# Performance work log

Hardware: AMD Instinct MI355X
Metric: run time of the kernel (lower is better)

The kernel has to match this reference:

```python
import jax, jax.numpy as jnp
import numpy as np

EPS = 1e-7  # keras_backend.epsilon()
ROUTINGS = 3


def setup_inputs() -> dict:
    key = jax.random.key(0)
    k1, k2, k3, k4, k5 = jax.random.split(key, 5)
    B, H, W, I, O = 32, 8, 8, 32, 64
    return {
        "inputs_poses": jax.random.normal(k1, (B, H, W, I, 4, 4), dtype=jnp.float32),
        "inputs_activations": jax.random.uniform(k2, (B, H, W, I), dtype=jnp.float32),
        "w": jax.random.normal(k3, (I, O, 4, 4), dtype=jnp.float32),
        "beta_v": jax.random.normal(k4, (1, O), dtype=jnp.float32),
        "beta_a": jax.random.normal(k5, (1, O), dtype=jnp.float32),
    }


def _em_routing(votes, i_act, beta_v, beta_a, routings):
    # votes: [B, N, O, 16], i_act: [B, N]
    B, N, O, P = votes.shape
    act = i_act[..., None, None]              # [B, N, 1, 1]
    bv = beta_v[..., None, :, None]           # [1, 1, O, 1]
    ba = beta_a[..., None, :, None]           # [1, 1, O, 1]
    rr = jnp.full((N, O, 1), 1.0 / O, dtype=votes.dtype)
    it_min, it_max = 1.0, min(routings, 3.0)
    o_mean = o_act = None
    for it in range(routings):
        inv_temp = it_min + (it_max - it_min) * it / max(1.0, routings - 1.0)
        # ---- m-step ----
        rr_prime = rr * act                                    # [B, N, O, 1]
        rps = rr_prime.sum(axis=-3, keepdims=True)             # [B, 1, O, 1]
        o_mean = (rr_prime * votes).sum(axis=-3, keepdims=True) / rps   # [B,1,O,16]
        o_stdv = jnp.sqrt((rr_prime * jnp.square(votes - o_mean)).sum(axis=-3, keepdims=True) / rps)
        o_cost_h = (bv + jnp.log(o_stdv + EPS)) * rps          # [B,1,O,16]
        o_cost = o_cost_h.sum(axis=-1, keepdims=True)          # [B,1,O,1]
        o_cost_mean = o_cost.mean(axis=-2, keepdims=True)      # [B,1,1,1]
        o_cost_stdv = jnp.sqrt(jnp.square(o_cost - o_cost_mean).sum(axis=-2, keepdims=True) / O)
        o_act = jax.nn.sigmoid(inv_temp * (ba + (o_cost_mean - o_cost) / (o_cost_stdv + EPS)))
        # ---- e-step ----
        if it < routings - 1:
            o_p = (-jnp.sum(jnp.square(votes - o_mean) / (2.0 * jnp.square(o_stdv)), axis=-1, keepdims=True)
                   - jnp.sum(jnp.log(o_stdv + EPS), axis=-1, keepdims=True))   # [B,N,O,1]
            zz = jnp.log(o_act + EPS) + o_p
            rr = jax.nn.softmax(zz, axis=-2)                   # softmax over O
    poses = jnp.squeeze(o_mean, axis=-3)                       # [B, O, 16]
    activations = jnp.squeeze(o_act, axis=(-3, -1))            # [B, O]
    return poses, activations


def reference(inputs_poses, inputs_activations, w, beta_v, beta_a):
    B, H, W, I = inputs_activations.shape
    O = w.shape[1]
    # mat_transform: per-(input-type, class) 4x4 pose transform -> votes
    pose = inputs_poses.reshape(B * H * W, I, 4, 4)
    votes = jnp.einsum('siab,iobc->sioac', pose, w)            # [BHW, I, O, 4, 4]
    votes = votes.reshape(B, H, W, I, O, 16)
    # coord_addition: add scaled spatial coords to components 0 (h) and 1 (w)
    ch = jnp.zeros((1, H, 1, 1, 1, 16), votes.dtype).at[..., 0].set(
        ((jnp.arange(H, dtype=votes.dtype) + 0.5) / H).reshape(1, H, 1, 1, 1))
    cw = jnp.zeros((1, 1, W, 1, 1, 16), votes.dtype).at[..., 1].set(
        ((jnp.arange(W, dtype=votes.dtype) + 0.5) / W).reshape(1, 1, W, 1, 1))
    votes = votes + ch + cw
    votes = votes.reshape(B, H * W * I, O, 16)
    i_act = inputs_activations.reshape(B, H * W * I)
    poses, activations = _em_routing(votes, i_act, beta_v, beta_a, ROUTINGS)
    poses = poses.reshape(B, O, 4, 4)
    return poses, activations
```

## Files before the change

kernel.cpp:

```cpp
#include <hip/hip_runtime.h>
#include <hip/hip_bf16.h>


#define NB 32
#define NN 2048
#define NO 64
#define NP 16
#define EPSF 1e-7f

#define SPB 4
#define NCHUNK 16
#define BLK_N (SPB * 32)

#define ACC_SLOTS 33
#define ACC_PER_B (ACC_SLOTS * NO)
#define PART_TOTAL (NB * NCHUNK * ACC_PER_B)

template <bool FIRST>
__global__ __launch_bounds__(1024) void accum_kernel(
    const float* __restrict__ pose,
    const float* __restrict__ act,
    const float* __restrict__ wmat,
    const float* __restrict__ stats,
    float* __restrict__ part)
{
    __shared__ float pose_s[BLK_N * 16];
    __shared__ float act_s[BLK_N];
    __shared__ float buf[SPB][ACC_PER_B];

    const int b = blockIdx.y;
    const int chunk = blockIdx.x;
    const int n0 = chunk * BLK_N;
    const int tid = threadIdx.x;

    {
        const float4* psrc = (const float4*)(pose + ((size_t)b * NN + n0) * 16);
        float4* pdst = (float4*)pose_s;
        if (tid < BLK_N * 4) pdst[tid] = psrc[tid];
        if (tid < BLK_N) act_s[tid] = act[(size_t)b * NN + n0 + tid];
    }
    __syncthreads();

    const int wv = tid >> 6;
    const int grp = wv >> 2;
    const int wvin = wv & 3;
    const int o = tid & 63;

    float m[16], i2v[16], zzb = 0.f;
    if (!FIRST) {
        const float* st = stats + (size_t)b * ACC_PER_B;
        #pragma unroll
        for (int p = 0; p < 16; p++) m[p] = st[p * 64 + o];
        #pragma unroll
        for (int p = 0; p < 16; p++) i2v[p] = st[(16 + p) * 64 + o];
        zzb = st[32 * 64 + o];
    }

    float accR = 0.f, acc1[16], acc2[16];
    #pragma unroll
    for (int p = 0; p < 16; p++) { acc1[p] = 0.f; acc2[p] = 0.f; }

    const int site = chunk * SPB + grp;
    const int hh = site >> 3, ww = site & 7;
    const float c0 = (hh + 0.5f) * 0.125f;
    const float c1 = (ww + 0.5f) * 0.125f;

    for (int ii = 0; ii < 8; ii++) {
        const int i = wvin * 8 + ii;
        const int nl = grp * 32 + i;
        const float4* wp = (const float4*)(wmat + ((size_t)i * 64 + o) * 16);
        float4 w0 = wp[0], w1 = wp[1], w2 = wp[2], w3 = wp[3];
        const float* pr = pose_s + nl * 16;
        float v[16];
        #pragma unroll
        for (int a = 0; a < 4; a++) {
            float pa0 = pr[a * 4 + 0], pa1 = pr[a * 4 + 1];
            float pa2 = pr[a * 4 + 2], pa3 = pr[a * 4 + 3];
            v[a * 4 + 0] = pa0 * w0.x + pa1 * w1.x + pa2 * w2.x + pa3 * w3.x;
            v[a * 4 + 1] = pa0 * w0.y + pa1 * w1.y + pa2 * w2.y + pa3 * w3.y;
            v[a * 4 + 2] = pa0 * w0.z + pa1 * w1.z + pa2 * w2.z + pa3 * w3.z;
            v[a * 4 + 3] = pa0 * w0.w + pa1 * w1.w + pa2 * w2.w + pa3 * w3.w;
        }
        v[0] += c0;
        v[1] += c1;

        float rr;
        if (FIRST) {
            rr = 1.0f / 64.0f;
        } else {
            float d = zzb;
            #pragma unroll
            for (int p = 0; p < 16; p++) {
                float t = v[p] - m[p];
                d -= t * t * i2v[p];
            }
            float mx = d;
            #pragma unroll
            for (int s = 32; s > 0; s >>= 1) mx = fmaxf(mx, __shfl_xor(mx, s, 64));
            float e = __expf(d - mx);
            float sum = e;
            #pragma unroll
            for (int s = 32; s > 0; s >>= 1) sum += __shfl_xor(sum, s, 64);
            rr = e / sum;
        }
        float rp = rr * act_s[nl];
        accR += rp;
        #pragma unroll
        for (int p = 0; p < 16; p++) {
            acc1[p] += rp * v[p];
            acc2[p] += rp * v[p] * v[p];
        }
    }

    if (wvin == 3) {
        float* r = buf[grp];
        r[32 * 64 + o] = accR;
        #pragma unroll
        for (int p = 0; p < 16; p++) r[p * 64 + o] = acc1[p];
        #pragma unroll
        for (int p = 0; p < 16; p++) r[(16 + p) * 64 + o] = acc2[p];
    }
    __syncthreads();
    if (wvin == 2) {
        float* r = buf[grp];
        r[32 * 64 + o] += accR;
        #pragma unroll
        for (int p = 0; p < 16; p++) r[p * 64 + o] += acc1[p];
        #pragma unroll
        for (int p = 0; p < 16; p++) r[(16 + p) * 64 + o] += acc2[p];
    }
    __syncthreads();
    if (wvin == 1) {
        float* r = buf[grp];
        r[32 * 64 + o] += accR;
        #pragma unroll
        for (int p = 0; p < 16; p++) r[p * 64 + o] += acc1[p];
        #pragma unroll
        for (int p = 0; p < 16; p++) r[(16 + p) * 64 + o] += acc2[p];
    }
    __syncthreads();
    if (wvin == 0) {
        float* r = buf[grp];
        r[32 * 64 + o] += accR;
        #pragma unroll
        for (int p = 0; p < 16; p++) r[p * 64 + o] += acc1[p];
        #pragma unroll
        for (int p = 0; p < 16; p++) r[(16 + p) * 64 + o] += acc2[p];
    }
    __syncthreads();

    float* pc = part + ((size_t)b * NCHUNK + chunk) * ACC_PER_B;
    for (int j = tid; j < ACC_PER_B; j += 1024)
        pc[j] = buf[0][j] + buf[1][j] + buf[2][j] + buf[3][j];
}

__global__ __launch_bounds__(256) void stats_kernel(
    const float* __restrict__ part,
    const float* __restrict__ beta_v,
    const float* __restrict__ beta_a,
    float* __restrict__ stats_out,
    float* __restrict__ out,
    float inv_temp)
{
    __shared__ float acc_s[ACC_PER_B];

    const int b = blockIdx.x;
    const int tid = threadIdx.x;

    {
        const float4* p4 = (const float4*)(part + (size_t)b * NCHUNK * ACC_PER_B);
        float4* a4 = (float4*)acc_s;
        for (int j = tid; j < ACC_PER_B / 4; j += 256) {
            float4 s = make_float4(0.f, 0.f, 0.f, 0.f);
            #pragma unroll
            for (int c = 0; c < NCHUNK; c++) {
                float4 v = p4[c * (ACC_PER_B / 4) + j];
                s.x += v.x; s.y += v.y; s.z += v.z; s.w += v.w;
            }
            a4[j] = s;
        }
    }
    __syncthreads();

    if (tid < 64) {
        const int o = tid;
        float rps = acc_s[32 * 64 + o];
        float m[16], var[16];
        float logsum = 0.f;
        #pragma unroll
        for (int p = 0; p < 16; p++) {
            float s1 = acc_s[p * 64 + o];
            float s2 = acc_s[(16 + p) * 64 + o];
            float mm = s1 / rps;
            float vv = fmaxf(s2 / rps - mm * mm, 0.f);
            m[p] = mm;
            var[p] = vv;
            logsum += __logf(sqrtf(vv) + EPSF);
        }
        float cost = rps * (16.0f * beta_v[o] + logsum);

        float cm = cost;
        #pragma unroll
        for (int s = 32; s > 0; s >>= 1) cm += __shfl_xor(cm, s, 64);
        cm *= (1.0f / 64.0f);
        float d = cost - cm;
        float cs = d * d;
        #pragma unroll
        for (int s = 32; s > 0; s >>= 1) cs += __shfl_xor(cs, s, 64);
        cs = sqrtf(cs * (1.0f / 64.0f));

        float x = inv_temp * (beta_a[o] + (cm - cost) / (cs + EPSF));
        float oa = 1.0f / (1.0f + __expf(-x));

        if (stats_out) {
            float* st = stats_out + (size_t)b * ACC_PER_B;
            #pragma unroll
            for (int p = 0; p < 16; p++) st[p * 64 + o] = m[p];
            #pragma unroll
            for (int p = 0; p < 16; p++) st[(16 + p) * 64 + o] = 0.5f / var[p];
            st[32 * 64 + o] = __logf(oa + EPSF) - logsum;
        }
        if (out) {
            float* op = out + ((size_t)b * 64 + o) * 16;
            #pragma unroll
            for (int p = 0; p < 16; p++) op[p] = m[p];
            out[(size_t)NB * NO * NP + (size_t)b * 64 + o] = oa;
        }
    }
}

extern "C" void kernel_launch(void* const* d_in, const int* in_sizes, int n_in,
                              void* d_out, int out_size, void* d_ws, size_t ws_size,
                              hipStream_t stream) {
    const float* pose   = (const float*)d_in[0];
    const float* act    = (const float*)d_in[1];
    const float* wmat   = (const float*)d_in[2];
    const float* beta_v = (const float*)d_in[3];
    const float* beta_a = (const float*)d_in[4];
    float* out = (float*)d_out;
    float* ws = (float*)d_ws;

    float* part   = ws;
    float* stats0 = ws + (size_t)PART_TOTAL;
    float* stats1 = stats0 + (size_t)NB * ACC_PER_B;

    dim3 grid(NCHUNK, NB);
    accum_kernel<true><<<grid, 1024, 0, stream>>>(pose, act, wmat, nullptr, part);
    stats_kernel<<<NB, 256, 0, stream>>>(part, beta_v, beta_a, stats0, nullptr, 1.0f);
    accum_kernel<false><<<grid, 1024, 0, stream>>>(pose, act, wmat, stats0, part);
    stats_kernel<<<NB, 256, 0, stream>>>(part, beta_v, beta_a, stats1, nullptr, 2.0f);
    accum_kernel<false><<<grid, 1024, 0, stream>>>(pose, act, wmat, stats1, part);
    stats_kernel<<<NB, 256, 0, stream>>>(part, beta_v, beta_a, nullptr, out, 3.0f);
}
```

Before: 171.4 us.

## Fuse intermediate stats computation into accumulation kernels and read poses directly

Removes the two intermediate stats kernels by having each block of the next accumulation pass reduce the previous pass's per-chunk partials and compute the mean, inverse variance and log-activation terms itself. Partial sums now ping-pong between two workspace buffers. Pose and activation values are read straight from global memory with wave-uniform indices instead of being staged in shared memory first. This cuts two kernel launches and their serialization, but each of the 16 chunk blocks per batch now repeats the same partial reduction and stats math redundantly.

```diff
diff --git a/kernel.cpp b/kernel.cpp
--- a/kernel.cpp
+++ b/kernel.cpp
@@ -1,5 +1,4 @@
 #include <hip/hip_runtime.h>
-#include <hip/hip_bf16.h>
 
 
 #define NB 32
@@ -14,72 +13,141 @@
 
 #define ACC_SLOTS 33
 #define ACC_PER_B (ACC_SLOTS * NO)
-#define PART_TOTAL (NB * NCHUNK * ACC_PER_B)
+#define PART_PER_BATCH (NCHUNK * ACC_PER_B)
+#define PART_TOTAL (NB * PART_PER_BATCH)
+
+__device__ __forceinline__ void reduce_store(
+    float buf[SPB][ACC_PER_B], int wvin, int grp, int o, int tid,
+    float accR, const float* acc1, const float* acc2, float* __restrict__ pc)
+{
+    if (wvin == 3) {
+        float* r = buf[grp];
+        r[32 * 64 + o] = accR;
+        #pragma unroll
+        for (int p = 0; p < 16; p++) r[p * 64 + o] = acc1[p];
+        #pragma unroll
+        for (int p = 0; p < 16; p++) r[(16 + p) * 64 + o] = acc2[p];
+    }
+    __syncthreads();
+    for (int round = 2; round >= 0; --round) {
+        if (wvin == round) {
+            float* r = buf[grp];
+            r[32 * 64 + o] += accR;
+            #pragma unroll
+            for (int p = 0; p < 16; p++) r[p * 64 + o] += acc1[p];
+            #pragma unroll
+            for (int p = 0; p < 16; p++) r[(16 + p) * 64 + o] += acc2[p];
+        }
+        __syncthreads();
+    }
+    for (int j = tid; j < ACC_PER_B; j += 1024)
+        pc[j] = buf[0][j] + buf[1][j] + buf[2][j] + buf[3][j];
+}
 
 template <bool FIRST>
 __global__ __launch_bounds__(1024) void accum_kernel(
     const float* __restrict__ pose,
     const float* __restrict__ act,
     const float* __restrict__ wmat,
-    const float* __restrict__ stats,
-    float* __restrict__ part)
+    const float* __restrict__ beta_v,
+    const float* __restrict__ beta_a,
+    const float* __restrict__ part_prev,
+    float* __restrict__ part_out,
+    float inv_temp)
 {
-    __shared__ float pose_s[BLK_N * 16];
-    __shared__ float act_s[BLK_N];
     __shared__ float buf[SPB][ACC_PER_B];
 
     const int b = blockIdx.y;
     const int chunk = blockIdx.x;
     const int n0 = chunk * BLK_N;
     const int tid = threadIdx.x;
-
-    {
-        const float4* psrc = (const float4*)(pose + ((size_t)b * NN + n0) * 16);
-        float4* pdst = (float4*)pose_s;
-        if (tid < BLK_N * 4) pdst[tid] = psrc[tid];
-        if (tid < BLK_N) act_s[tid] = act[(size_t)b * NN + n0 + tid];
-    }
-    __syncthreads();
-
-    const int wv = tid >> 6;
-    const int grp = wv >> 2;
-    const int wvin = wv & 3;
-    const int o = tid & 63;
+    const int wv = tid >> 6, grp = wv >> 2, wvin = wv & 3, o = tid & 63;
 
     float m[16], i2v[16], zzb = 0.f;
     if (!FIRST) {
-        const float* st = stats + (size_t)b * ACC_PER_B;
-        #pragma unroll
-        for (int p = 0; p < 16; p++) m[p] = st[p * 64 + o];
-        #pragma unroll
-        for (int p = 0; p < 16; p++) i2v[p] = st[(16 + p) * 64 + o];
-        zzb = st[32 * 64 + o];
-    }
+        float* sb = buf[0];
+        {
+            const float4* p4 = (const float4*)(part_prev + (size_t)b * PART_PER_BATCH);
+            float4* a4 = (float4*)sb;
+            for (int j = tid; j < ACC_PER_B / 4; j += 1024) {
+                float4 s = make_float4(0.f, 0.f, 0.f, 0.f);
+                #pragma unroll
+                for (int c = 0; c < NCHUNK; c++) {
+                    float4 vv = p4[c * (ACC_PER_B / 4) + j];
+                    s.x += vv.x; s.y += vv.y; s.z += vv.z; s.w += vv.w;
+                }
+                a4[j] = s;
+            }
+        }
+        __syncthreads();
+        if (tid < 64) {
+            float rps = sb[32 * 64 + o];
+            float mm[16], var[16];
+            float logsum = 0.f;
+            #pragma unroll
+            for (int p = 0; p < 16; p++) {
+                float s1 = sb[p * 64 + o];
+                float s2 = sb[(16 + p) * 64 + o];
+                float mv = s1 / rps;
+                float vv = fmaxf(s2 / rps - mv * mv, 0.f);
+                mm[p] = mv;
+                var[p] = vv;
+                logsum += __logf(sqrtf(vv) + EPSF);
+            }
+            float cost = rps * (16.0f * beta_v[o] + logsum);
+            float cm = cost;
+            #pragma unroll
+            for (int s = 32; s > 0; s >>= 1) cm += __shfl_xor(cm, s, 64);
+            cm *= (1.0f / 64.0f);
+            float dd = cost - cm;
+            float cs = dd * dd;
+            #pragma unroll
+            for (int s = 32; s > 0; s >>= 1) cs += __shfl_xor(cs, s, 64);
+            cs = sqrtf(cs * (1.0f / 64.0f));
+            float x = inv_temp * (beta_a[o] + (cm - cost) / (cs + EPSF));
+            float oa = 1.0f / (1.0f + __expf(-x));
+            #pragma unroll
+            for (int p = 0; p < 16; p++) sb[p * 64 + o] = mm[p];
+            #pragma unroll
+            for (int p = 0; p < 16; p++) sb[(16 + p) * 64 + o] = 0.5f / var[p];
+            sb[32 * 64 + o] = __logf(oa + EPSF) - logsum;
+        }
+        __syncthreads();
+        #pragma unroll
+        for (int p = 0; p < 16; p++) m[p] = sb[p * 64 + o];
+        #pragma unroll
+        for (int p = 0; p < 16; p++) i2v[p] = sb[(16 + p) * 64 + o];
+        zzb = sb[32 * 64 + o];
+        __syncthreads();
+    }
+
+    const float* pose_b = pose + ((size_t)b * NN + n0) * 16;
+    const float* act_b  = act + (size_t)b * NN + n0;
+    const int site = chunk * SPB + grp;
+    const float c0 = ((site >> 3) + 0.5f) * 0.125f;
+    const float c1 = ((site & 7) + 0.5f) * 0.125f;
 
     float accR = 0.f, acc1[16], acc2[16];
     #pragma unroll
     for (int p = 0; p < 16; p++) { acc1[p] = 0.f; acc2[p] = 0.f; }
 
-    const int site = chunk * SPB + grp;
-    const int hh = site >> 3, ww = site & 7;
-    const float c0 = (hh + 0.5f) * 0.125f;
-    const float c1 = (ww + 0.5f) * 0.125f;
-
     for (int ii = 0; ii < 8; ii++) {
         const int i = wvin * 8 + ii;
-        const int nl = grp * 32 + i;
+        const int nl = __builtin_amdgcn_readfirstlane(grp * 32 + i);
+        const float4* pr4 = (const float4*)(pose_b + (size_t)nl * 16);
+        const float av = act_b[nl];
+
         const float4* wp = (const float4*)(wmat + ((size_t)i * 64 + o) * 16);
         float4 w0 = wp[0], w1 = wp[1], w2 = wp[2], w3 = wp[3];
-        const float* pr = pose_s + nl * 16;
+
         float v[16];
         #pragma unroll
         for (int a = 0; a < 4; a++) {
-            float pa0 = pr[a * 4 + 0], pa1 = pr[a * 4 + 1];
-            float pa2 = pr[a * 4 + 2], pa3 = pr[a * 4 + 3];
-            v[a * 4 + 0] = pa0 * w0.x + pa1 * w1.x + pa2 * w2.x + pa3 * w3.x;
-            v[a * 4 + 1] = pa0 * w0.y + pa1 * w1.y + pa2 * w2.y + pa3 * w3.y;
-            v[a * 4 + 2] = pa0 * w0.z + pa1 * w1.z + pa2 * w2.z + pa3 * w3.z;
-            v[a * 4 + 3] = pa0 * w0.w + pa1 * w1.w + pa2 * w2.w + pa3 * w3.w;
+            float4 pa = pr4[a];
+            v[a * 4 + 0] = pa.x * w0.x + pa.y * w1.x + pa.z * w2.x + pa.w * w3.x;
+            v[a * 4 + 1] = pa.x * w0.y + pa.y * w1.y + pa.z * w2.y + pa.w * w3.y;
+            v[a * 4 + 2] = pa.x * w0.z + pa.y * w1.z + pa.z * w2.z + pa.w * w3.z;
+            v[a * 4 + 3] = pa.x * w0.w + pa.y * w1.w + pa.z * w2.w + pa.w * w3.w;
         }
         v[0] += c0;
         v[1] += c1;
@@ -103,7 +171,7 @@
             for (int s = 32; s > 0; s >>= 1) sum += __shfl_xor(sum, s, 64);
             rr = e / sum;
         }
-        float rp = rr * act_s[nl];
+        float rp = rr * av;
         accR += rp;
         #pragma unroll
         for (int p = 0; p < 16; p++) {
@@ -112,53 +180,14 @@
         }
     }
 
-    if (wvin == 3) {
-        float* r = buf[grp];
-        r[32 * 64 + o] = accR;
-        #pragma unroll
-        for (int p = 0; p < 16; p++) r[p * 64 + o] = acc1[p];
-        #pragma unroll
-        for (int p = 0; p < 16; p++) r[(16 + p) * 64 + o] = acc2[p];
-    }
-    __syncthreads();
-    if (wvin == 2) {
-        float* r = buf[grp];
-        r[32 * 64 + o] += accR;
-        #pragma unroll
-        for (int p = 0; p < 16; p++) r[p * 64 + o] += acc1[p];
-        #pragma unroll
-        for (int p = 0; p < 16; p++) r[(16 + p) * 64 + o] += acc2[p];
-    }
-    __syncthreads();
-    if (wvin == 1) {
-        float* r = buf[grp];
-        r[32 * 64 + o] += accR;
-        #pragma unroll
-        for (int p = 0; p < 16; p++) r[p * 64 + o] += acc1[p];
-        #pragma unroll
-        for (int p = 0; p < 16; p++) r[(16 + p) * 64 + o] += acc2[p];
-    }
-    __syncthreads();
-    if (wvin == 0) {
-        float* r = buf[grp];
-        r[32 * 64 + o] += accR;
-        #pragma unroll
-        for (int p = 0; p < 16; p++) r[p * 64 + o] += acc1[p];
-        #pragma unroll
-        for (int p = 0; p < 16; p++) r[(16 + p) * 64 + o] += acc2[p];
-    }
-    __syncthreads();
-
-    float* pc = part + ((size_t)b * NCHUNK + chunk) * ACC_PER_B;
-    for (int j = tid; j < ACC_PER_B; j += 1024)
-        pc[j] = buf[0][j] + buf[1][j] + buf[2][j] + buf[3][j];
-}
-
-__global__ __launch_bounds__(256) void stats_kernel(
+    float* pc = part_out + ((size_t)b * NCHUNK + chunk) * ACC_PER_B;
+    reduce_store(buf, wvin, grp, o, tid, accR, acc1, acc2, pc);
+}
+
+__global__ __launch_bounds__(256) void stats_final(
     const float* __restrict__ part,
     const float* __restrict__ beta_v,
     const float* __restrict__ beta_a,
-    float* __restrict__ stats_out,
     float* __restrict__ out,
     float inv_temp)
 {
@@ -168,14 +197,14 @@
     const int tid = threadIdx.x;
 
     {
-        const float4* p4 = (const float4*)(part + (size_t)b * NCHUNK * ACC_PER_B);
+        const float4* p4 = (const float4*)(part + (size_t)b * PART_PER_BATCH);
         float4* a4 = (float4*)acc_s;
         for (int j = tid; j < ACC_PER_B / 4; j += 256) {
             float4 s = make_float4(0.f, 0.f, 0.f, 0.f);
             #pragma unroll
             for (int c = 0; c < NCHUNK; c++) {
-                float4 v = p4[c * (ACC_PER_B / 4) + j];
-                s.x += v.x; s.y += v.y; s.z += v.z; s.w += v.w;
+                float4 vv = p4[c * (ACC_PER_B / 4) + j];
+                s.x += vv.x; s.y += vv.y; s.z += vv.z; s.w += vv.w;
             }
             a4[j] = s;
         }
@@ -185,7 +214,7 @@
     if (tid < 64) {
         const int o = tid;
         float rps = acc_s[32 * 64 + o];
-        float m[16], var[16];
+        float m[16];
         float logsum = 0.f;
         #pragma unroll
         for (int p = 0; p < 16; p++) {
@@ -194,7 +223,6 @@
             float mm = s1 / rps;
             float vv = fmaxf(s2 / rps - mm * mm, 0.f);
             m[p] = mm;
-            var[p] = vv;
             logsum += __logf(sqrtf(vv) + EPSF);
         }
         float cost = rps * (16.0f * beta_v[o] + logsum);
@@ -203,8 +231,8 @@
         #pragma unroll
         for (int s = 32; s > 0; s >>= 1) cm += __shfl_xor(cm, s, 64);
         cm *= (1.0f / 64.0f);
-        float d = cost - cm;
-        float cs = d * d;
+        float dd = cost - cm;
+        float cs = dd * dd;
         #pragma unroll
         for (int s = 32; s > 0; s >>= 1) cs += __shfl_xor(cs, s, 64);
         cs = sqrtf(cs * (1.0f / 64.0f));
@@ -212,20 +240,10 @@
         float x = inv_temp * (beta_a[o] + (cm - cost) / (cs + EPSF));
         float oa = 1.0f / (1.0f + __expf(-x));
 
-        if (stats_out) {
-            float* st = stats_out + (size_t)b * ACC_PER_B;
-            #pragma unroll
-            for (int p = 0; p < 16; p++) st[p * 64 + o] = m[p];
-            #pragma unroll
-            for (int p = 0; p < 16; p++) st[(16 + p) * 64 + o] = 0.5f / var[p];
-            st[32 * 64 + o] = __logf(oa + EPSF) - logsum;
-        }
-        if (out) {
-            float* op = out + ((size_t)b * 64 + o) * 16;
-            #pragma unroll
-            for (int p = 0; p < 16; p++) op[p] = m[p];
-            out[(size_t)NB * NO * NP + (size_t)b * 64 + o] = oa;
-        }
+        float* op = out + ((size_t)b * 64 + o) * 16;
+        #pragma unroll
+        for (int p = 0; p < 16; p++) op[p] = m[p];
+        out[(size_t)NB * NO * NP + (size_t)b * 64 + o] = oa;
     }
 }
 
@@ -240,15 +258,15 @@
     float* out = (float*)d_out;
     float* ws = (float*)d_ws;
 
-    float* part   = ws;
-    float* stats0 = ws + (size_t)PART_TOTAL;
-    float* stats1 = stats0 + (size_t)NB * ACC_PER_B;
+    float* pA = ws;
+    float* pB = ws + (size_t)PART_TOTAL;
 
     dim3 grid(NCHUNK, NB);
-    accum_kernel<true><<<grid, 1024, 0, stream>>>(pose, act, wmat, nullptr, part);
-    stats_kernel<<<NB, 256, 0, stream>>>(part, beta_v, beta_a, stats0, nullptr, 1.0f);
-    accum_kernel<false><<<grid, 1024, 0, stream>>>(pose, act, wmat, stats0, part);
-    stats_kernel<<<NB, 256, 0, stream>>>(part, beta_v, beta_a, stats1, nullptr, 2.0f);
-    accum_kernel<false><<<grid, 1024, 0, stream>>>(pose, act, wmat, stats1, part);
-    stats_kernel<<<NB, 256, 0, stream>>>(part, beta_v, beta_a, nullptr, out, 3.0f);
-}
+    accum_kernel<true ><<<grid, 1024, 0, stream>>>(pose, act, wmat, beta_v, beta_a,
+                                                   nullptr, pA, 0.0f);
+    accum_kernel<false><<<grid, 1024, 0, stream>>>(pose, act, wmat, beta_v, beta_a,
+                                                   pA, pB, 1.0f);
+    accum_kernel<false><<<grid, 1024, 0, stream>>>(pose, act, wmat, beta_v, beta_a,
+                                                   pB, pA, 2.0f);
+    stats_final<<<NB, 256, 0, stream>>>(pA, beta_v, beta_a, out, 3.0f);
+}
```

Measured after the change: 170.8 us. Within noise of the previous version (-0.3%).
